# Kernel tuning notes

Hardware: AMD Instinct MI355X
Metric: run time of the kernel (lower is better)

The kernel has to match this reference:

```python
import jax, jax.numpy as jnp
import numpy as np

N_STEPS = 10
DT = 0.01
TAU = 0.1
LAM = 0.1


def setup_inputs() -> dict:
    key = jax.random.key(0)
    k1, k2 = jax.random.split(key)
    x = jax.random.normal(k1, (4, 2048, 1024), dtype=jnp.float32)
    W = jax.random.normal(k2, (1024, 4096), dtype=jnp.float32) * 0.02
    return {"x": x, "W": W}


def reference(x, W):
    orig_shape = x.shape
    D = orig_shape[-1]
    x_flat = x.reshape(-1, D)                      # [N, d_model]
    b = x_flat @ W                                 # [N, d_lca]
    G = W.T @ W                                    # [d_lca, d_lca]
    G = G - jnp.diag(jnp.diag(G))                  # zero self-inhibition
    u0 = jnp.zeros_like(b)

    def step(u, _):
        a = jax.nn.relu(u - LAM)
        du = (b - a @ G - u) / TAU
        return u + DT * du, None

    u, _ = jax.lax.scan(step, u0, None, length=N_STEPS)
    a = jax.nn.relu(u - LAM)
    out = a @ W.T                                  # [N, d_model]
    return out.reshape(orig_shape)
```

## Files before the change

### kernel.cpp

```cpp
#include <hip/hip_runtime.h>
#include <hip/hip_bf16.h>


typedef __bf16 bf16_t;
typedef __bf16 bf16x8 __attribute__((ext_vector_type(8)));
typedef __bf16 bf16x4 __attribute__((ext_vector_type(4)));
typedef float  f32x4  __attribute__((ext_vector_type(4)));

__device__ __forceinline__ void g2lds16(const void* g, void* l) {
    __builtin_amdgcn_global_load_lds(
        (const __attribute__((address_space(1))) void*)g,
        (__attribute__((address_space(3))) void*)l,
        16, 0, 0);
}

template<int N> __device__ __forceinline__ void waitv() {
    if constexpr (N == 0) asm volatile("s_waitcnt vmcnt(0)" ::: "memory");
    else if constexpr (N == 1) asm volatile("s_waitcnt vmcnt(1)" ::: "memory");
    else if constexpr (N == 2) asm volatile("s_waitcnt vmcnt(2)" ::: "memory");
    else if constexpr (N == 3) asm volatile("s_waitcnt vmcnt(3)" ::: "memory");
    else if constexpr (N == 4) asm volatile("s_waitcnt vmcnt(4)" ::: "memory");
    else if constexpr (N == 5) asm volatile("s_waitcnt vmcnt(5)" ::: "memory");
    else if constexpr (N == 6) asm volatile("s_waitcnt vmcnt(6)" ::: "memory");
}
__device__ __forceinline__ void bar() { __builtin_amdgcn_s_barrier(); }

template<int n> struct IC { static constexpr int v = n; };

enum { MODE_B = 0, MODE_T = 1, MODE_STEP2 = 2, MODE_OUT = 3 };

template<int MODE, int BM>
__global__ __launch_bounds__(512, 2)
void gemm_bt(const bf16_t* __restrict__ A, const bf16_t* __restrict__ Bt,
             int N, int K,
             float*  __restrict__ outF,
             bf16_t* __restrict__ outH,
             bf16_t* __restrict__ bb,
             bf16_t* __restrict__ u,
             const float* __restrict__ g)
{
    constexpr int BN  = 256;
    constexpr int FM  = BM / 32;
    constexpr int FMH = FM / 2;
    constexpr int AUH = BM / 128;
    constexpr int ASZ = BM * 128;
    constexpr int BSZ = BN * 128;

    __shared__ __attribute__((aligned(16))) bf16_t As[2 * BM * 64];
    __shared__ __attribute__((aligned(16))) bf16_t Bs[2 * BN * 64];

    const int t = threadIdx.x;
    const int l = t & 63;
    const int w = t >> 6;
    const int wm = (w >> 2) * (BM / 4);
    const int wn = (w & 3) * 32;

    const int gx  = gridDim.x;
    const int nwg = gx * gridDim.y;
    const int bid = blockIdx.y * gx + blockIdx.x;
    const int sw  = (bid & 7) * (nwg >> 3) + (bid >> 3);
    const int rowA = (sw / gx) * BM;
    const int colB = (sw % gx) * BN;

    const int srow = t >> 3;
    const int scol = (((t & 7) ^ (srow & 7)) << 3);
    const bf16_t* gA = A  + (size_t)(rowA + srow) * K + scol;
    const bf16_t* gB = Bt + (size_t)(colB + srow) * K + scol;
    char* sA = (char*)As + t * 16;
    char* sB = (char*)Bs + t * 16;

    auto stA = [&](int slot, int kt, int uu) {
        g2lds16(gA + (size_t)uu * 64 * K + kt * 64, sA + slot * ASZ + uu * 8192);
    };
    auto stB = [&](int slot, int kt, int uu) {
        g2lds16(gB + (size_t)uu * 64 * K + kt * 64, sB + slot * BSZ + uu * 8192);
    };

    const int lrow = l & 15;
    const int c0 = ((l >> 4) << 4) ^ ((l & 7) << 4);
    const char* cAs = (const char*)As;
    const char* cBs = (const char*)Bs;
    auto rdA = [&](int slot, int qi, int ii, int p) {
        return (const bf16x8*)(cAs + slot * ASZ
            + (size_t)(qi * (BM / 2) + wm + ii * 16 + lrow) * 128 + (c0 ^ (p << 6)));
    };
    auto rdB = [&](int slot, int qj, int jj, int p) {
        return (const bf16x8*)(cBs + slot * BSZ
            + (size_t)(qj * 128 + wn + jj * 16 + lrow) * 128 + (c0 ^ (p << 6)));
    };

    f32x4 acc[FM][4];
#pragma unroll
    for (int i = 0; i < FM; ++i)
#pragma unroll
        for (int j = 0; j < 4; ++j)
#pragma unroll
            for (int r = 0; r < 4; ++r) acc[i][j][r] = 0.f;

    auto tile = [&](auto W0, auto W1, auto W2, int slot, int ktN, bool st) {
        const int ns = slot ^ 1;
        bf16x8 af[FMH][2], bf0[2][2], bf1[2][2];
        if (st) { stB(ns, ktN, 0); stB(ns, ktN, 1); }
        waitv<decltype(W0)::v>(); bar();
#pragma unroll
        for (int ii = 0; ii < FMH; ++ii)
#pragma unroll
            for (int p = 0; p < 2; ++p) af[ii][p] = *rdA(slot, 0, ii, p);
#pragma unroll
        for (int jj = 0; jj < 2; ++jj)
#pragma unroll
            for (int p = 0; p < 2; ++p) bf0[jj][p] = *rdB(slot, 0, jj, p);
        __builtin_amdgcn_s_setprio(1);
#pragma unroll
        for (int ii = 0; ii < FMH; ++ii)
#pragma unroll
            for (int jj = 0; jj < 2; ++jj)
#pragma unroll
                for (int p = 0; p < 2; ++p)
                    acc[ii][jj] = __builtin_amdgcn_mfma_f32_16x16x32_bf16(
                        bf0[jj][p], af[ii][p], acc[ii][jj], 0, 0, 0);
        __builtin_amdgcn_s_setprio(0);
        if (st) { stA(ns, ktN, 0); if constexpr (AUH == 2) stA(ns, ktN, 1); }
        waitv<decltype(W1)::v>(); bar();
#pragma unroll
        for (int jj = 0; jj < 2; ++jj)
#pragma unroll
            for (int p = 0; p < 2; ++p) bf1[jj][p] = *rdB(slot, 1, jj, p);
        __builtin_amdgcn_s_setprio(1);
#pragma unroll
        for (int ii = 0; ii < FMH; ++ii)
#pragma unroll
            for (int jj = 0; jj < 2; ++jj)
#pragma unroll
                for (int p = 0; p < 2; ++p)
                    acc[ii][2 + jj] = __builtin_amdgcn_mfma_f32_16x16x32_bf16(
                        bf1[jj][p], af[ii][p], acc[ii][2 + jj], 0, 0, 0);
        __builtin_amdgcn_s_setprio(0);
        if (st) { stB(ns, ktN, 2); stB(ns, ktN, 3); }
        waitv<decltype(W2)::v>(); bar();
#pragma unroll
        for (int ii = 0; ii < FMH; ++ii)
#pragma unroll
            for (int p = 0; p < 2; ++p) af[ii][p] = *rdA(slot, 1, ii, p);
        __builtin_amdgcn_s_setprio(1);
#pragma unroll
        for (int ii = 0; ii < FMH; ++ii)
#pragma unroll
            for (int jj = 0; jj < 2; ++jj)
#pragma unroll
                for (int p = 0; p < 2; ++p)
                    acc[FMH + ii][2 + jj] = __builtin_amdgcn_mfma_f32_16x16x32_bf16(
                        bf1[jj][p], af[ii][p], acc[FMH + ii][2 + jj], 0, 0, 0);
        __builtin_amdgcn_s_setprio(0);
        if (st) { stA(ns, ktN, AUH); if constexpr (AUH == 2) stA(ns, ktN, 3); }
        __builtin_amdgcn_s_setprio(1);
#pragma unroll
        for (int ii = 0; ii < FMH; ++ii)
#pragma unroll
            for (int jj = 0; jj < 2; ++jj)
#pragma unroll
                for (int p = 0; p < 2; ++p)
                    acc[FMH + ii][jj] = __builtin_amdgcn_mfma_f32_16x16x32_bf16(
                        bf0[jj][p], af[ii][p], acc[FMH + ii][jj], 0, 0, 0);
        __builtin_amdgcn_s_setprio(0);
    };

    stB(0, 0, 0); stB(0, 0, 1);
    stA(0, 0, 0); if constexpr (AUH == 2) stA(0, 0, 1);
    stB(0, 0, 2); stB(0, 0, 3);
    stA(0, 0, AUH); if constexpr (AUH == 2) stA(0, 0, 3);

    const int NT = K >> 6;
    for (int kt = 0; kt < NT - 1; ++kt) {
        if constexpr (BM == 256) tile(IC<6>{}, IC<6>{}, IC<6>{}, kt & 1, kt + 1, true);
        else                     tile(IC<5>{}, IC<4>{}, IC<5>{}, kt & 1, kt + 1, true);
    }
    if constexpr (BM == 256) tile(IC<4>{}, IC<2>{}, IC<0>{}, (NT - 1) & 1, 0, false);
    else                     tile(IC<3>{}, IC<1>{}, IC<0>{}, (NT - 1) & 1, 0, false);

    const int m0 = rowA + wm + lrow;
    const int n0 = colB + wn + ((l >> 4) * 4);

    f32x4 gvv[4];
    if constexpr (MODE == MODE_STEP2) {
#pragma unroll
        for (int j = 0; j < 4; ++j)
            gvv[j] = *(const f32x4*)(g + n0 + (j & 1) * 16 + (j >> 1) * 128);
    }

#pragma unroll
    for (int i = 0; i < FM; ++i) {
        const int m = m0 + (i & (FMH - 1)) * 16 + (i / FMH) * (BM / 2);
#pragma unroll
        for (int j = 0; j < 4; ++j) {
            const size_t idx = (size_t)m * N + (n0 + (j & 1) * 16 + (j >> 1) * 128);
            const f32x4 c = acc[i][j];
            if constexpr (MODE == MODE_T) {
                bf16x4 o;
#pragma unroll
                for (int r = 0; r < 4; ++r) o[r] = (bf16_t)c[r];
                *(bf16x4*)(outH + idx) = o;
            } else if constexpr (MODE == MODE_B) {
                bf16x4 ob, ou, oa;
#pragma unroll
                for (int r = 0; r < 4; ++r) {
                    const float un = 0.1f * c[r];
                    ob[r] = (bf16_t)c[r];
                    ou[r] = (bf16_t)un;
                    oa[r] = (bf16_t)fmaxf(un - 0.1f, 0.f);
                }
                *(bf16x4*)(bb   + idx) = ob;
                *(bf16x4*)(u    + idx) = ou;
                *(bf16x4*)(outH + idx) = oa;
            } else if constexpr (MODE == MODE_STEP2) {
                const bf16x4 uv = *(const bf16x4*)(u  + idx);
                const bf16x4 bv = *(const bf16x4*)(bb + idx);
                bf16x4 ou, oa;
#pragma unroll
                for (int r = 0; r < 4; ++r) {
                    const float uo = (float)uv[r];
                    const float ao = fmaxf(uo - 0.1f, 0.f);
                    const float un = 0.9f * uo + 0.1f * (float)bv[r]
                                   - 0.1f * c[r] + 0.1f * ao * gvv[j][r];
                    ou[r] = (bf16_t)un;
                    oa[r] = (bf16_t)fmaxf(un - 0.1f, 0.f);
                }
                *(bf16x4*)(u    + idx) = ou;
                *(bf16x4*)(outH + idx) = oa;
            } else {
                *(f32x4*)(outF + idx) = c;
            }
        }
    }
}

__global__ void cast_x_kernel(const float* __restrict__ x, bf16_t* __restrict__ xh, int n) {
    int i = blockIdx.x * 256 + threadIdx.x;
    if (i < n) xh[i] = (bf16_t)x[i];
}

__global__ void prep_w_kernel(const float* __restrict__ W,
                              bf16_t* __restrict__ Wh, bf16_t* __restrict__ WT) {
    int i = blockIdx.x * 256 + threadIdx.x;
    if (i < 1024 * 4096) {
        int k = i >> 12;
        int n = i & 4095;
        bf16_t v = (bf16_t)W[i];
        Wh[i] = v;
        WT[(size_t)n * 1024 + k] = v;
    }
}

__global__ void prep_g_kernel(const float* __restrict__ W, float* __restrict__ g) {
    int j = blockIdx.x * 256 + threadIdx.x;
    if (j < 4096) {
        float s = 0.f;
        for (int k = 0; k < 1024; ++k) {
            float v = W[(size_t)k * 4096 + j];
            s += v * v;
        }
        g[j] = s;
    }
}

extern "C" void kernel_launch(void* const* d_in, const int* in_sizes, int n_in,
                              void* d_out, int out_size, void* d_ws, size_t ws_size,
                              hipStream_t stream)
{
    const float* x = (const float*)d_in[0];
    const float* W = (const float*)d_in[1];

    bf16_t* xh = (bf16_t*)d_out;
    bf16_t* tt = (bf16_t*)d_out;
    float*  gd = (float*)((char*)d_out + 16777216);

    char* ws = (char*)d_ws;
    bf16_t* a  = (bf16_t*)(ws);
    bf16_t* bb = (bf16_t*)(ws + 67108864);
    bf16_t* u  = (bf16_t*)(ws + 134217728);
    bf16_t* Wh = (bf16_t*)(ws + 201326592);
    bf16_t* WT = (bf16_t*)(ws + 209715200);

    cast_x_kernel<<<8388608 / 256, 256, 0, stream>>>(x, xh, 8388608);
    prep_w_kernel<<<4194304 / 256, 256, 0, stream>>>(W, Wh, WT);
    prep_g_kernel<<<16, 256, 0, stream>>>(W, gd);

    gemm_bt<MODE_B, 256><<<dim3(16, 32), 512, 0, stream>>>(xh, WT, 4096, 1024,
                                                           nullptr, a, bb, u, nullptr);
    for (int s = 0; s < 9; ++s) {
        gemm_bt<MODE_T, 128><<<dim3(4, 64), 512, 0, stream>>>(a, Wh, 1024, 4096,
                                                              nullptr, tt, nullptr, nullptr, nullptr);
        gemm_bt<MODE_STEP2, 256><<<dim3(16, 32), 512, 0, stream>>>(tt, WT, 4096, 1024,
                                                                   nullptr, a, bb, u, gd);
    }
    gemm_bt<MODE_OUT, 128><<<dim3(4, 64), 512, 0, stream>>>(a, Wh, 1024, 4096,
                                                            (float*)d_out, nullptr, nullptr, nullptr, nullptr);
}
```

Measured before the change: 2.056 ms.

## Fuse relu activation into A-operand load of small GEMMs, drop activation buffer

```diff
diff --git a/kernel.cpp b/kernel.cpp
--- a/kernel.cpp
+++ b/kernel.cpp
@@ -24,6 +24,9 @@
     else if constexpr (N == 6) asm volatile("s_waitcnt vmcnt(6)" ::: "memory");
 }
 __device__ __forceinline__ void bar() { __builtin_amdgcn_s_barrier(); }
+__device__ __forceinline__ void waitlgkm0() {
+    asm volatile("s_waitcnt lgkmcnt(0)" ::: "memory");
+}
 
 template<int n> struct IC { static constexpr int v = n; };
 
@@ -42,11 +45,10 @@
     constexpr int BN  = 256;
     constexpr int FM  = BM / 32;
     constexpr int FMH = FM / 2;
-    constexpr int AUH = BM / 128;
     constexpr int ASZ = BM * 128;
     constexpr int BSZ = BN * 128;
 
-    __shared__ __attribute__((aligned(16))) bf16_t As[2 * BM * 64];
+    __shared__ __attribute__((aligned(16))) bf16_t As[(BM == 256 ? 2 : 1) * BM * 64];
     __shared__ __attribute__((aligned(16))) bf16_t Bs[2 * BN * 64];
 
     const int t = threadIdx.x;
@@ -64,14 +66,8 @@
 
     const int srow = t >> 3;
     const int scol = (((t & 7) ^ (srow & 7)) << 3);
-    const bf16_t* gA = A  + (size_t)(rowA + srow) * K + scol;
     const bf16_t* gB = Bt + (size_t)(colB + srow) * K + scol;
-    char* sA = (char*)As + t * 16;
     char* sB = (char*)Bs + t * 16;
-
-    auto stA = [&](int slot, int kt, int uu) {
-        g2lds16(gA + (size_t)uu * 64 * K + kt * 64, sA + slot * ASZ + uu * 8192);
-    };
     auto stB = [&](int slot, int kt, int uu) {
         g2lds16(gB + (size_t)uu * 64 * K + kt * 64, sB + slot * BSZ + uu * 8192);
     };
@@ -97,86 +93,196 @@
 #pragma unroll
             for (int r = 0; r < 4; ++r) acc[i][j][r] = 0.f;
 
-    auto tile = [&](auto W0, auto W1, auto W2, int slot, int ktN, bool st) {
-        const int ns = slot ^ 1;
-        bf16x8 af[FMH][2], bf0[2][2], bf1[2][2];
-        if (st) { stB(ns, ktN, 0); stB(ns, ktN, 1); }
-        waitv<decltype(W0)::v>(); bar();
-#pragma unroll
-        for (int ii = 0; ii < FMH; ++ii)
-#pragma unroll
-            for (int p = 0; p < 2; ++p) af[ii][p] = *rdA(slot, 0, ii, p);
-#pragma unroll
-        for (int jj = 0; jj < 2; ++jj)
-#pragma unroll
-            for (int p = 0; p < 2; ++p) bf0[jj][p] = *rdB(slot, 0, jj, p);
-        __builtin_amdgcn_s_setprio(1);
-#pragma unroll
-        for (int ii = 0; ii < FMH; ++ii)
+    const int NT = K >> 6;
+
+    if constexpr (BM == 256) {
+        const bf16_t* gA = A + (size_t)(rowA + srow) * K + scol;
+        char* sA = (char*)As + t * 16;
+        auto stA = [&](int slot, int kt, int uu) {
+            g2lds16(gA + (size_t)uu * 64 * K + kt * 64, sA + slot * ASZ + uu * 8192);
+        };
+
+        auto tile = [&](auto W0, auto W1, auto W2, int slot, int ktN, bool st) {
+            const int ns = slot ^ 1;
+            bf16x8 af[FMH][2], bf0[2][2], bf1[2][2];
+            if (st) { stB(ns, ktN, 0); stB(ns, ktN, 1); }
+            waitv<decltype(W0)::v>(); bar();
+#pragma unroll
+            for (int ii = 0; ii < FMH; ++ii)
+#pragma unroll
+                for (int p = 0; p < 2; ++p) af[ii][p] = *rdA(slot, 0, ii, p);
 #pragma unroll
             for (int jj = 0; jj < 2; ++jj)
 #pragma unroll
-                for (int p = 0; p < 2; ++p)
-                    acc[ii][jj] = __builtin_amdgcn_mfma_f32_16x16x32_bf16(
-                        bf0[jj][p], af[ii][p], acc[ii][jj], 0, 0, 0);
-        __builtin_amdgcn_s_setprio(0);
-        if (st) { stA(ns, ktN, 0); if constexpr (AUH == 2) stA(ns, ktN, 1); }
-        waitv<decltype(W1)::v>(); bar();
-#pragma unroll
-        for (int jj = 0; jj < 2; ++jj)
-#pragma unroll
-            for (int p = 0; p < 2; ++p) bf1[jj][p] = *rdB(slot, 1, jj, p);
-        __builtin_amdgcn_s_setprio(1);
-#pragma unroll
-        for (int ii = 0; ii < FMH; ++ii)
+                for (int p = 0; p < 2; ++p) bf0[jj][p] = *rdB(slot, 0, jj, p);
+            __builtin_amdgcn_s_setprio(1);
+#pragma unroll
+            for (int ii = 0; ii < FMH; ++ii)
+#pragma unroll
+                for (int jj = 0; jj < 2; ++jj)
+#pragma unroll
+                    for (int p = 0; p < 2; ++p)
+                        acc[ii][jj] = __builtin_amdgcn_mfma_f32_16x16x32_bf16(
+                            bf0[jj][p], af[ii][p], acc[ii][jj], 0, 0, 0);
+            __builtin_amdgcn_s_setprio(0);
+            if (st) { stA(ns, ktN, 0); stA(ns, ktN, 1); }
+            waitv<decltype(W1)::v>(); bar();
 #pragma unroll
             for (int jj = 0; jj < 2; ++jj)
 #pragma unroll
-                for (int p = 0; p < 2; ++p)
-                    acc[ii][2 + jj] = __builtin_amdgcn_mfma_f32_16x16x32_bf16(
-                        bf1[jj][p], af[ii][p], acc[ii][2 + jj], 0, 0, 0);
-        __builtin_amdgcn_s_setprio(0);
-        if (st) { stB(ns, ktN, 2); stB(ns, ktN, 3); }
-        waitv<decltype(W2)::v>(); bar();
-#pragma unroll
-        for (int ii = 0; ii < FMH; ++ii)
-#pragma unroll
-            for (int p = 0; p < 2; ++p) af[ii][p] = *rdA(slot, 1, ii, p);
-        __builtin_amdgcn_s_setprio(1);
-#pragma unroll
-        for (int ii = 0; ii < FMH; ++ii)
+                for (int p = 0; p < 2; ++p) bf1[jj][p] = *rdB(slot, 1, jj, p);
+            __builtin_amdgcn_s_setprio(1);
+#pragma unroll
+            for (int ii = 0; ii < FMH; ++ii)
+#pragma unroll
+                for (int jj = 0; jj < 2; ++jj)
+#pragma unroll
+                    for (int p = 0; p < 2; ++p)
+                        acc[ii][2 + jj] = __builtin_amdgcn_mfma_f32_16x16x32_bf16(
+                            bf1[jj][p], af[ii][p], acc[ii][2 + jj], 0, 0, 0);
+            __builtin_amdgcn_s_setprio(0);
+            if (st) { stB(ns, ktN, 2); stB(ns, ktN, 3); }
+            waitv<decltype(W2)::v>(); bar();
+#pragma unroll
+            for (int ii = 0; ii < FMH; ++ii)
+#pragma unroll
+                for (int p = 0; p < 2; ++p) af[ii][p] = *rdA(slot, 1, ii, p);
+            __builtin_amdgcn_s_setprio(1);
+#pragma unroll
+            for (int ii = 0; ii < FMH; ++ii)
+#pragma unroll
+                for (int jj = 0; jj < 2; ++jj)
+#pragma unroll
+                    for (int p = 0; p < 2; ++p)
+                        acc[FMH + ii][2 + jj] = __builtin_amdgcn_mfma_f32_16x16x32_bf16(
+                            bf1[jj][p], af[ii][p], acc[FMH + ii][2 + jj], 0, 0, 0);
+            __builtin_amdgcn_s_setprio(0);
+            if (st) { stA(ns, ktN, 2); stA(ns, ktN, 3); }
+            __builtin_amdgcn_s_setprio(1);
+#pragma unroll
+            for (int ii = 0; ii < FMH; ++ii)
+#pragma unroll
+                for (int jj = 0; jj < 2; ++jj)
+#pragma unroll
+                    for (int p = 0; p < 2; ++p)
+                        acc[FMH + ii][jj] = __builtin_amdgcn_mfma_f32_16x16x32_bf16(
+                            bf0[jj][p], af[ii][p], acc[FMH + ii][jj], 0, 0, 0);
+            __builtin_amdgcn_s_setprio(0);
+        };
+
+        stB(0, 0, 0); stB(0, 0, 1);
+        stA(0, 0, 0); stA(0, 0, 1);
+        stB(0, 0, 2); stB(0, 0, 3);
+        stA(0, 0, 2); stA(0, 0, 3);
+
+        for (int kt = 0; kt < NT - 1; ++kt)
+            tile(IC<6>{}, IC<6>{}, IC<6>{}, kt & 1, kt + 1, true);
+        tile(IC<4>{}, IC<2>{}, IC<0>{}, (NT - 1) & 1, 0, false);
+    } else {
+        const int s_arow = t >> 3;
+        const int s_acb  = ((t & 7) << 4) ^ ((s_arow & 7) << 4);
+        const bf16_t* gAr = A + (size_t)(rowA + s_arow) * K + (t & 7) * 8;
+        auto reluv = [&](bf16x8 v) {
+            bf16x8 r;
+#pragma unroll
+            for (int e = 0; e < 8; ++e)
+                r[e] = (bf16_t)fmaxf((float)v[e] - 0.1f, 0.f);
+            return r;
+        };
+        auto wrA = [&](bf16x8 v, int gg) {
+            *(bf16x8*)((char*)As + (size_t)(gg * 64 + s_arow) * 128 + s_acb) = v;
+        };
+
+        {
+            bf16x8 a0 = *(const bf16x8*)(gAr);
+            bf16x8 a1 = *(const bf16x8*)(gAr + (size_t)64 * K);
+            waitv<0>();
+            wrA(reluv(a0), 0);
+            wrA(reluv(a1), 1);
+            waitlgkm0();
+            stB(0, 0, 0); stB(0, 0, 1); stB(0, 0, 2); stB(0, 0, 3);
+        }
+
+        for (int kt = 0; kt < NT; ++kt) {
+            const bool st = (kt + 1 < NT);
+            const int slot = kt & 1, ns = slot ^ 1;
+            bf16x8 af[FMH][2], bf0[2][2], bf1[2][2];
+            bf16x8 nA0, nA1;
+            if (st) {
+                nA0 = *(const bf16x8*)(gAr + (kt + 1) * 64);
+                nA1 = *(const bf16x8*)(gAr + (size_t)64 * K + (kt + 1) * 64);
+            }
+            if (st) waitv<4>(); else waitv<2>();
+            bar();
+#pragma unroll
+            for (int ii = 0; ii < FMH; ++ii)
+#pragma unroll
+                for (int p = 0; p < 2; ++p) af[ii][p] = *rdA(0, 0, ii, p);
 #pragma unroll
             for (int jj = 0; jj < 2; ++jj)
 #pragma unroll
-                for (int p = 0; p < 2; ++p)
-                    acc[FMH + ii][2 + jj] = __builtin_amdgcn_mfma_f32_16x16x32_bf16(
-                        bf1[jj][p], af[ii][p], acc[FMH + ii][2 + jj], 0, 0, 0);
-        __builtin_amdgcn_s_setprio(0);
-        if (st) { stA(ns, ktN, AUH); if constexpr (AUH == 2) stA(ns, ktN, 3); }
-        __builtin_amdgcn_s_setprio(1);
-#pragma unroll
-        for (int ii = 0; ii < FMH; ++ii)
+                for (int p = 0; p < 2; ++p) bf0[jj][p] = *rdB(slot, 0, jj, p);
+            __builtin_amdgcn_s_setprio(1);
+#pragma unroll
+            for (int ii = 0; ii < FMH; ++ii)
+#pragma unroll
+                for (int jj = 0; jj < 2; ++jj)
+#pragma unroll
+                    for (int p = 0; p < 2; ++p)
+                        acc[ii][jj] = __builtin_amdgcn_mfma_f32_16x16x32_bf16(
+                            bf0[jj][p], af[ii][p], acc[ii][jj], 0, 0, 0);
+            __builtin_amdgcn_s_setprio(0);
+            if (st) { stB(ns, kt + 1, 0); stB(ns, kt + 1, 1); }
+            if (st) waitv<4>(); else waitv<0>();
+            bar();
 #pragma unroll
             for (int jj = 0; jj < 2; ++jj)
 #pragma unroll
-                for (int p = 0; p < 2; ++p)
-                    acc[FMH + ii][jj] = __builtin_amdgcn_mfma_f32_16x16x32_bf16(
-                        bf0[jj][p], af[ii][p], acc[FMH + ii][jj], 0, 0, 0);
-        __builtin_amdgcn_s_setprio(0);
-    };
-
-    stB(0, 0, 0); stB(0, 0, 1);
-    stA(0, 0, 0); if constexpr (AUH == 2) stA(0, 0, 1);
-    stB(0, 0, 2); stB(0, 0, 3);
-    stA(0, 0, AUH); if constexpr (AUH == 2) stA(0, 0, 3);
-
-    const int NT = K >> 6;
-    for (int kt = 0; kt < NT - 1; ++kt) {
-        if constexpr (BM == 256) tile(IC<6>{}, IC<6>{}, IC<6>{}, kt & 1, kt + 1, true);
-        else                     tile(IC<5>{}, IC<4>{}, IC<5>{}, kt & 1, kt + 1, true);
-    }
-    if constexpr (BM == 256) tile(IC<4>{}, IC<2>{}, IC<0>{}, (NT - 1) & 1, 0, false);
-    else                     tile(IC<3>{}, IC<1>{}, IC<0>{}, (NT - 1) & 1, 0, false);
+                for (int p = 0; p < 2; ++p) bf1[jj][p] = *rdB(slot, 1, jj, p);
+            __builtin_amdgcn_s_setprio(1);
+#pragma unroll
+            for (int ii = 0; ii < FMH; ++ii)
+#pragma unroll
+                for (int jj = 0; jj < 2; ++jj)
+#pragma unroll
+                    for (int p = 0; p < 2; ++p)
+                        acc[ii][2 + jj] = __builtin_amdgcn_mfma_f32_16x16x32_bf16(
+                            bf1[jj][p], af[ii][p], acc[ii][2 + jj], 0, 0, 0);
+            __builtin_amdgcn_s_setprio(0);
+            if (st) { stB(ns, kt + 1, 2); stB(ns, kt + 1, 3); }
+#pragma unroll
+            for (int ii = 0; ii < FMH; ++ii)
+#pragma unroll
+                for (int p = 0; p < 2; ++p) af[ii][p] = *rdA(0, 1, ii, p);
+            __builtin_amdgcn_s_setprio(1);
+#pragma unroll
+            for (int ii = 0; ii < FMH; ++ii)
+#pragma unroll
+                for (int jj = 0; jj < 2; ++jj)
+#pragma unroll
+                    for (int p = 0; p < 2; ++p)
+                        acc[FMH + ii][2 + jj] = __builtin_amdgcn_mfma_f32_16x16x32_bf16(
+                            bf1[jj][p], af[ii][p], acc[FMH + ii][2 + jj], 0, 0, 0);
+            __builtin_amdgcn_s_setprio(0);
+            bar();
+            if (st) {
+                waitv<4>();
+                wrA(reluv(nA0), 0);
+                wrA(reluv(nA1), 1);
+                waitlgkm0();
+            }
+            __builtin_amdgcn_s_setprio(1);
+#pragma unroll
+            for (int ii = 0; ii < FMH; ++ii)
+#pragma unroll
+                for (int jj = 0; jj < 2; ++jj)
+#pragma unroll
+                    for (int p = 0; p < 2; ++p)
+                        acc[FMH + ii][jj] = __builtin_amdgcn_mfma_f32_16x16x32_bf16(
+                            bf0[jj][p], af[ii][p], acc[FMH + ii][jj], 0, 0, 0);
+            __builtin_amdgcn_s_setprio(0);
+        }
+    }
 
     const int m0 = rowA + wm + lrow;
     const int n0 = colB + wn + ((l >> 4) * 4);
@@ -201,21 +307,19 @@
                 for (int r = 0; r < 4; ++r) o[r] = (bf16_t)c[r];
                 *(bf16x4*)(outH + idx) = o;
             } else if constexpr (MODE == MODE_B) {
-                bf16x4 ob, ou, oa;
+                bf16x4 ob, ou;
 #pragma unroll
                 for (int r = 0; r < 4; ++r) {
                     const float un = 0.1f * c[r];
                     ob[r] = (bf16_t)c[r];
                     ou[r] = (bf16_t)un;
-                    oa[r] = (bf16_t)fmaxf(un - 0.1f, 0.f);
                 }
-                *(bf16x4*)(bb   + idx) = ob;
-                *(bf16x4*)(u    + idx) = ou;
-                *(bf16x4*)(outH + idx) = oa;
+                *(bf16x4*)(bb + idx) = ob;
+                *(bf16x4*)(u  + idx) = ou;
             } else if constexpr (MODE == MODE_STEP2) {
                 const bf16x4 uv = *(const bf16x4*)(u  + idx);
                 const bf16x4 bv = *(const bf16x4*)(bb + idx);
-                bf16x4 ou, oa;
+                bf16x4 ou;
 #pragma unroll
                 for (int r = 0; r < 4; ++r) {
                     const float uo = (float)uv[r];
@@ -223,10 +327,8 @@
                     const float un = 0.9f * uo + 0.1f * (float)bv[r]
                                    - 0.1f * c[r] + 0.1f * ao * gvv[j][r];
                     ou[r] = (bf16_t)un;
-                    oa[r] = (bf16_t)fmaxf(un - 0.1f, 0.f);
                 }
-                *(bf16x4*)(u    + idx) = ou;
-                *(bf16x4*)(outH + idx) = oa;
+                *(bf16x4*)(u + idx) = ou;
             } else {
                 *(f32x4*)(outF + idx) = c;
             }
@@ -275,7 +377,6 @@
     float*  gd = (float*)((char*)d_out + 16777216);
 
     char* ws = (char*)d_ws;
-    bf16_t* a  = (bf16_t*)(ws);
     bf16_t* bb = (bf16_t*)(ws + 67108864);
     bf16_t* u  = (bf16_t*)(ws + 134217728);
     bf16_t* Wh = (bf16_t*)(ws + 201326592);
@@ -286,13 +387,13 @@
     prep_g_kernel<<<16, 256, 0, stream>>>(W, gd);
 
     gemm_bt<MODE_B, 256><<<dim3(16, 32), 512, 0, stream>>>(xh, WT, 4096, 1024,
-                                                           nullptr, a, bb, u, nullptr);
+                                                           nullptr, nullptr, bb, u, nullptr);
     for (int s = 0; s < 9; ++s) {
-        gemm_bt<MODE_T, 128><<<dim3(4, 64), 512, 0, stream>>>(a, Wh, 1024, 4096,
+        gemm_bt<MODE_T, 128><<<dim3(4, 64), 512, 0, stream>>>(u, Wh, 1024, 4096,
                                                               nullptr, tt, nullptr, nullptr, nullptr);
         gemm_bt<MODE_STEP2, 256><<<dim3(16, 32), 512, 0, stream>>>(tt, WT, 4096, 1024,
-                                                                   nullptr, a, bb, u, gd);
-    }
-    gemm_bt<MODE_OUT, 128><<<dim3(4, 64), 512, 0, stream>>>(a, Wh, 1024, 4096,
+                                                                   nullptr, nullptr, bb, u, gd);
+    }
+    gemm_bt<MODE_OUT, 128><<<dim3(4, 64), 512, 0, stream>>>(u, Wh, 1024, 4096,
                                                             (float*)d_out, nullptr, nullptr, nullptr, nullptr);
 }
```

After: 2.037 ms. No clear change (-0.9%).
